# Optimization experiments

Hardware: AMD Instinct MI355X
Metric: run time of the kernel (lower is better)

The kernel has to match this reference:

```python
import jax, jax.numpy as jnp
import numpy as np
from jax import lax

B, C, H, W = 64, 512, 20, 15
N = H * W  # must be 300 (ChannelAttention dim)
EPS = 1e-5


def layernorm(x, w, b):
    m = x.mean(-1, keepdims=True)
    v = x.var(-1, keepdims=True)
    return (x - m) * lax.rsqrt(v + EPS) * w + b


def batchnorm(x, w, b):  # training-mode BN over (B,H,W), x: (B,C,H,W)
    m = x.mean((0, 2, 3), keepdims=True)
    v = x.var((0, 2, 3), keepdims=True)
    return (x - m) * lax.rsqrt(v + EPS) * w[None, :, None, None] + b[None, :, None, None]


def cross_linear_attn(x1, x2, kv1_w, kv2_w, heads):
    # x: (B, n, c); kv_w: (2c, c). Linear-attention variant: softmax over channel axis of k^T v.
    b, n, c = x1.shape
    d = c // heads
    scale = d ** -0.5

    def split_q(x):
        return x.reshape(b, n, heads, d).transpose(0, 2, 1, 3)  # (b,h,n,d)

    def kv(x, w):
        t = (x @ w.T).reshape(b, n, 2, heads, d).transpose(2, 0, 3, 1, 4)
        return t[0], t[1]  # each (b,h,n,d)

    q1, q2 = split_q(x1), split_q(x2)
    k1, v1 = kv(x1, kv1_w)
    k2, v2 = kv(x2, kv2_w)

    def ctx(k, v):  # (b,h,d,d), softmax over dim -2
        return jax.nn.softmax(jnp.einsum('bhnd,bhne->bhde', k, v) * scale, axis=-2)

    c1, c2 = ctx(k1, v1), ctx(k2, v2)

    def out(q, cx):
        return jnp.einsum('bhnd,bhde->bhne', q, cx).transpose(0, 2, 1, 3).reshape(b, n, c)

    return out(q1, c2), out(q2, c1)  # cross: q1 uses ctx2, q2 uses ctx1


def conv1x1(x, w):  # x: (B,Ci,H,W), w: (Co,Ci)
    return jnp.einsum('oi,bihw->bohw', w, x)


def setup_inputs() -> dict:
    key = jax.random.key(0)
    ks = jax.random.split(key, 24)
    g = lambda i, shape, s=0.02: jax.random.normal(ks[i], shape, jnp.float32) * s
    inp = {
        'x1': jax.random.normal(ks[0], (B, C, H, W), jnp.float32),
        'x2': jax.random.normal(ks[1], (B, C, H, W), jnp.float32),
        # CrossPath channel_proj1/2: Linear(C, 2C) + LayerNorm(2C)
        'cp1_w': g(2, (2 * C, C)), 'cp1_b': jnp.zeros((2 * C,), jnp.float32),
        'ln1_w': jnp.ones((2 * C,), jnp.float32), 'ln1_b': jnp.zeros((2 * C,), jnp.float32),
        'cp2_w': g(3, (2 * C, C)), 'cp2_b': jnp.zeros((2 * C,), jnp.float32),
        'ln2_w': jnp.ones((2 * C,), jnp.float32), 'ln2_b': jnp.zeros((2 * C,), jnp.float32),
        # SpatialAttention (dim=C, heads=8) kv linears, no bias
        's_kv1_w': g(4, (2 * C, C)), 's_kv2_w': g(5, (2 * C, C)),
        # ChannelAttention (dim=N=300, heads=4) kv linears, no bias
        'c_kv1_w': g(6, (2 * N, N)), 'c_kv2_w': g(7, (2 * N, N)),
        # ChannelEmbed(2C -> C)
        'res_w': g(8, (C, 2 * C), np.sqrt(2.0 / C)),
        'ce1_w': g(9, (C, 2 * C), np.sqrt(2.0 / C)), 'ce1_b': jnp.zeros((C,), jnp.float32),
        'dw_w': g(10, (C, 1, 3, 3), np.sqrt(2.0 / 9.0)), 'dw_b': jnp.zeros((C,), jnp.float32),
        'ce3_w': g(11, (C, C), np.sqrt(2.0 / C)), 'ce3_b': jnp.zeros((C,), jnp.float32),
        'bn_e_w': jnp.ones((C,), jnp.float32), 'bn_e_b': jnp.zeros((C,), jnp.float32),
        'bn_o_w': jnp.ones((C,), jnp.float32), 'bn_o_b': jnp.zeros((C,), jnp.float32),
    }
    return inp


def reference(x1, x2, cp1_w, cp1_b, ln1_w, ln1_b, cp2_w, cp2_b, ln2_w, ln2_b,
              s_kv1_w, s_kv2_w, c_kv1_w, c_kv2_w,
              res_w, ce1_w, ce1_b, dw_w, dw_b, ce3_w, ce3_b,
              bn_e_w, bn_e_b, bn_o_w, bn_o_b):
    b, c, h, w = x1.shape
    n = h * w
    t1 = x1.reshape(b, c, n).transpose(0, 2, 1)  # (B,N,C)
    t2 = x2.reshape(b, c, n).transpose(0, 2, 1)

    a1 = jax.nn.relu(layernorm(t1 @ cp1_w.T + cp1_b, ln1_w, ln1_b))
    a2 = jax.nn.relu(layernorm(t2 @ cp2_w.T + cp2_b, ln2_w, ln2_b))
    c1, s1 = a1[..., :c], a1[..., c:]
    c2, s2 = a2[..., :c], a2[..., c:]

    v1, v2 = cross_linear_attn(s1, s2, s_kv1_w, s_kv2_w, heads=8)
    z1, z2 = cross_linear_attn(c1.transpose(0, 2, 1), c2.transpose(0, 2, 1),
                               c_kv1_w, c_kv2_w, heads=4)
    s = v1 + v2                                  # (B,N,C)
    cc = (z1 + z2).transpose(0, 2, 1)            # (B,N,C)

    merge = jnp.concatenate([s, cc], axis=-1)    # (B,N,2C)
    xm = merge.transpose(0, 2, 1).reshape(b, 2 * c, h, w)

    residual = conv1x1(xm, res_w)
    e = conv1x1(xm, ce1_w) + ce1_b[None, :, None, None]
    e = lax.conv_general_dilated(e, dw_w, (1, 1), 'SAME',
                                 dimension_numbers=('NCHW', 'OIHW', 'NCHW'),
                                 feature_group_count=c) + dw_b[None, :, None, None]
    e = jnp.where(e >= 0, e, 0.01 * e)  # LeakyReLU(0.01)
    e = conv1x1(e, ce3_w) + ce3_b[None, :, None, None]
    e = batchnorm(e, bn_e_w, bn_e_b)
    return batchnorm(residual + e, bn_o_w, bn_o_b)
```

## Files before the change

### kernel.cpp

```cpp
#include <hip/hip_runtime.h>

typedef unsigned short u16;
typedef __attribute__((ext_vector_type(8))) short bh8;
typedef __attribute__((ext_vector_type(4))) float f4;

__device__ __forceinline__ u16 f2b(float f){
  unsigned int u = __float_as_uint(f);
  u += 0x7fffu + ((u >> 16) & 1u);
  return (u16)(u >> 16);
}
__device__ __forceinline__ float b2f(u16 h){
  return __uint_as_float(((unsigned int)h) << 16);
}
__device__ __forceinline__ void gl16(const u16* g, u16* l){
  __builtin_amdgcn_global_load_lds((const __attribute__((address_space(1))) void*)g,
                                   (__attribute__((address_space(3))) void*)l, 16, 0, 0);
}

__global__ void pack_plain(const float* __restrict__ src, u16* __restrict__ dst, int count){
  int i = blockIdx.x*256 + threadIdx.x;
  if (i < count) dst[i] = f2b(src[i]);
}
__global__ void pack_ckv_k(const float* __restrict__ src, u16* __restrict__ dst){
  int i = blockIdx.x*256 + threadIdx.x;
  int nn = i / 320, kk = i - (i/320)*320;
  int t_ = (nn >= 320) ? 1 : 0;
  int rem = nn - t_*320;
  int hh = rem / 80, dd = rem - hh*80;
  int kh = kk / 80, kd = kk - kh*80;
  float v = 0.f;
  if (dd < 75 && kd < 75)
    v = src[(size_t)(t_*300 + hh*75 + dd)*300 + (kh*75 + kd)];
  dst[i] = f2b(v);
}
__global__ void pack_dw(const float* __restrict__ src, u16* __restrict__ dst){
  int i = blockIdx.x*256 + threadIdx.x;
  if (i < 4608){
    int t = i >> 9, c = i & 511;
    dst[i] = f2b(src[c*9 + t]);
  }
}
__global__ void pad_zero(u16* __restrict__ slack){
  const int j = blockIdx.x*256 + threadIdx.x;
  if (j < 2048) slack[j] = 0;
}

__global__ __launch_bounds__(256)
void transpose_k(const float* __restrict__ x, u16* __restrict__ t)
{
  __shared__ float tile[32][33];
  const int n0 = blockIdx.x * 32, c0 = blockIdx.y * 32, b = blockIdx.z;
  const int ln = threadIdx.x & 31, lr = threadIdx.x >> 5;
  #pragma unroll
  for (int q = 0; q < 4; q++) {
    const int c = c0 + lr + q*8, n = n0 + ln;
    tile[lr + q*8][ln] = (n < 300) ? x[((long)b*512 + c)*300 + n] : 0.f;
  }
  __syncthreads();
  #pragma unroll
  for (int q = 0; q < 4; q++) {
    const int n = n0 + lr + q*8;
    if (n < 300) t[((long)b*300 + n)*512 + c0 + ln] = f2b(tile[ln][lr + q*8]);
  }
}

template<int OUTF, int HASB>
__global__ __launch_bounds__(512)
void gemm_k(const u16* __restrict__ A, int lda,
            const u16* __restrict__ Bw, const u16* __restrict__ Bw2, int ldb, long mhalf,
            u16* __restrict__ Cb, float* __restrict__ Cf, int ldc,
            const float* __restrict__ bias, const float* __restrict__ bias2, int K)
{
  __shared__ u16 As[3][8192];
  __shared__ u16 Bs[3][4096];
  const int tid = threadIdx.x;
  const int gx = gridDim.x;
  const int nwg = gx * gridDim.y;
  const int flat = blockIdx.y * gx + blockIdx.x;
  const int qq = nwg >> 3, rr = nwg & 7, xcd = flat & 7, lin = flat >> 3;
  const int newid = (xcd < rr ? xcd*(qq+1) : rr*(qq+1) + (xcd-rr)*qq) + lin;
  const long n0 = (long)(newid % gx) * 128;
  const long m0 = (long)(newid / gx) * 256;
  const u16* Bwp = Bw; const float* bp = bias;
  if (Bw2 != nullptr && m0 >= mhalf){ Bwp = Bw2; bp = bias2; }
  const int wave = tid >> 6, lane = tid & 63;
  const int l15 = lane & 15, lg = lane >> 4;
  const int wr = (wave >> 1) * 64, wc = (wave & 1) * 64;
  const int arow = tid >> 2;
  const int aseg = ((tid & 3) ^ ((arow >> 1) & 3)) * 8;
  const u16* Ag0 = A + (m0 + arow) * (long)lda + aseg;
  const u16* Ag1 = A + (m0 + 128 + arow) * (long)lda + aseg;
  const u16* Bg0 = Bwp + (n0 + arow) * (long)ldb + aseg;
  const int to8 = tid * 8;
  int roA[4], roB[4];
  #pragma unroll
  for (int i = 0; i < 4; i++){
    const int rA = wr + i*16 + l15;
    roA[i] = rA*32 + ((lg ^ ((rA >> 1) & 3)) * 8);
    const int rB = wc + i*16 + l15;
    roB[i] = rB*32 + ((lg ^ ((rB >> 1) & 3)) * 8);
  }
  f4 acc[4][4] = {};
  const int NT = K >> 5;
  {
    gl16(Ag0, &As[0][to8]); gl16(Ag1, &As[0][4096 + to8]); gl16(Bg0, &Bs[0][to8]);
    gl16(Ag0 + 32, &As[1][to8]); gl16(Ag1 + 32, &As[1][4096 + to8]); gl16(Bg0 + 32, &Bs[1][to8]);
  }
  int rd = 0;
  for (int t = 0; t < NT; t++) {
    if (t < NT - 1) { asm volatile("s_waitcnt vmcnt(3)" ::: "memory"); }
    else            { asm volatile("s_waitcnt vmcnt(0)" ::: "memory"); }
    __builtin_amdgcn_sched_barrier(0);
    __builtin_amdgcn_s_barrier();
    __builtin_amdgcn_sched_barrier(0);
    if (t + 2 < NT) {
      int wb = rd + 2; if (wb >= 3) wb -= 3;
      const int kt = (t + 2) << 5;
      gl16(Ag0 + kt, &As[wb][to8]); gl16(Ag1 + kt, &As[wb][4096 + to8]); gl16(Bg0 + kt, &Bs[wb][to8]);
    }
    bh8 af[4], bf[4];
    #pragma unroll
    for (int mi = 0; mi < 4; mi++) af[mi] = *(const bh8*)&As[rd][roA[mi]];
    #pragma unroll
    for (int ni = 0; ni < 4; ni++) bf[ni] = *(const bh8*)&Bs[rd][roB[ni]];
    #pragma unroll
    for (int mi = 0; mi < 4; mi++)
      #pragma unroll
      for (int ni = 0; ni < 4; ni++)
        acc[mi][ni] = __builtin_amdgcn_mfma_f32_16x16x32_bf16(af[mi], bf[ni], acc[mi][ni], 0, 0, 0);
    rd++; if (rd == 3) rd = 0;
  }
  if (OUTF == 2) {
    if (n0 < 512) {
      #pragma unroll
      for (int ni = 0; ni < 4; ni++) {
        const long cn = n0 + wc + ni*16 + l15;
        #pragma unroll
        for (int mi = 0; mi < 4; mi++)
          #pragma unroll
          for (int r = 0; r < 4; r++) {
            const long cm = m0 + wr + mi*16 + lg*4 + r;
            Cf[cm * ldc + cn] = acc[mi][ni][r];
          }
      }
    } else {
      #pragma unroll
      for (int ni = 0; ni < 4; ni++) {
        const long cn = n0 - 512 + wc + ni*16 + l15;
        const float bv = bias[cn];
        #pragma unroll
        for (int mi = 0; mi < 4; mi++)
          #pragma unroll
          for (int r = 0; r < 4; r++) {
            const long cm = m0 + wr + mi*16 + lg*4 + r;
            Cb[cm * ldc + cn] = f2b(acc[mi][ni][r] + bv);
          }
      }
    }
  } else {
    #pragma unroll
    for (int ni = 0; ni < 4; ni++) {
      const long cn = n0 + wc + ni*16 + l15;
      const float bv = HASB ? bp[cn] : 0.0f;
      #pragma unroll
      for (int mi = 0; mi < 4; mi++) {
        #pragma unroll
        for (int r = 0; r < 4; r++) {
          const long cm = m0 + wr + mi*16 + lg*4 + r;
          const float v = acc[mi][ni][r] + bv;
          if (OUTF) Cf[cm * ldc + cn] = v;
          else      Cb[cm * ldc + cn] = f2b(v);
        }
      }
    }
  }
}

__global__ __launch_bounds__(256)
void ln_kernel(const u16* __restrict__ apre, const float* __restrict__ lw, const float* __restrict__ lb,
               u16* __restrict__ s, u16* __restrict__ cT)
{
  __shared__ u16 tile[40][520];
  const int bh = blockIdx.x;
  const int b = bh >> 2, h = bh & 3;
  const int z = blockIdx.y;
  const int dd0 = z ? 40 : 0;
  const int ndd = z ? 35 : 40;
  const int segbase = z ? 5 : 0;
  const int tid = threadIdx.x, w = tid >> 6, lane = tid & 63;
  const int r0 = b*300 + h*75 + dd0;
  for (int dl = w; dl < ndd; dl += 4){
    const int r = r0 + dl;
    const u16* row = apre + (size_t)r*1024 + lane*8;
    const bh8 vc = *(const bh8*)row;
    const bh8 vs = *(const bh8*)(row + 512);
    float fc[8], fs[8];
    float sm = 0.f, sq = 0.f;
    #pragma unroll
    for (int j = 0; j < 8; j++){
      fc[j] = b2f((u16)vc[j]); fs[j] = b2f((u16)vs[j]);
      sm += fc[j] + fs[j];
      sq += fc[j]*fc[j] + fs[j]*fs[j];
    }
    #pragma unroll
    for (int o = 32; o; o >>= 1){ sm += __shfl_xor(sm, o); sq += __shfl_xor(sq, o); }
    const float mean = sm * (1.f/1024.f);
    const float rstd = rsqrtf(sq*(1.f/1024.f) - mean*mean + 1e-5f);
    bh8 oc, os;
    #pragma unroll
    for (int j = 0; j < 8; j++){
      const int c = lane*8 + j;
      const float y1 = (fc[j]-mean)*rstd*lw[c] + lb[c];
      oc[j] = (short)f2b(fmaxf(y1, 0.f));
      const float y2 = (fs[j]-mean)*rstd*lw[512+c] + lb[512+c];
      os[j] = (short)f2b(fmaxf(y2, 0.f));
    }
    *(bh8*)&tile[dl][lane*8] = oc;
    *(bh8*)&s[(size_t)r*512 + lane*8] = os;
  }
  __syncthreads();
  for (int i = tid; i < 2560; i += 256){
    const int c = i / 5, sg = i - (i/5)*5;
    const int seg = segbase + sg;
    bh8 ov;
    #pragma unroll
    for (int j = 0; j < 8; j++){
      const int dl = seg*8 + j - dd0;
      ov[j] = (short)((dl >= 0 && dl < ndd) ? tile[dl][c] : (u16)0);
    }
    *(bh8*)&cT[((size_t)b*512 + c)*320 + h*80 + seg*8] = ov;
  }
}

template<int D, int DREAL, int OS>
__global__ __launch_bounds__(256)
void ctx_kernel(const u16* __restrict__ kva, const u16* __restrict__ kvb,
                u16* __restrict__ outp, int K, int RS, int VOFF, float scale)
{
  constexpr int NT = D/16, MT = D/16, MTL = (MT+3)/4, SEG = D/8;
  __shared__ u16 vT[D][40];
  __shared__ u16 kT[D][40];
  const int h = blockIdx.x, b = blockIdx.y, iq = blockIdx.z;
  const int Hn = gridDim.x;
  const u16* base = (iq ? kvb : kva) + (size_t)b*K*RS + h*D;
  u16* out = outp + (((size_t)iq*64 + b)*Hn + h)*(size_t)(D*OS);
  const int tid = threadIdx.x, w = tid >> 6, lane = tid & 63, l15 = lane & 15, lg = lane >> 4;
  f4 acc[MTL][NT] = {};
  for (int k0 = 0; k0 < K; k0 += 32) {
    __syncthreads();
    for (int sI = tid; sI < 32*SEG; sI += 256) {
      const int nn = sI / SEG, dseg = sI - (sI/SEG)*SEG;
      bh8 kk = {}, vv = {};
      const int krow = k0 + nn;
      if (krow < K) {
        const u16* p = base + (size_t)krow*RS + dseg*8;
        kk = *(const bh8*)p;
        vv = *(const bh8*)(p + VOFF);
      }
      #pragma unroll
      for (int j = 0; j < 8; j++){
        kT[dseg*8+j][nn] = (u16)kk[j];
        vT[dseg*8+j][nn] = (u16)vv[j];
      }
    }
    __syncthreads();
    #pragma unroll
    for (int ii = 0; ii < MTL; ii++){
      const int mt = w + ii*4;
      if (MT % 4 != 0 && mt >= MT) break;
      const bh8 a = *(const bh8*)&vT[mt*16 + l15][lg*8];
      #pragma unroll
      for (int nt = 0; nt < NT; nt++){
        const bh8 bb = *(const bh8*)&kT[nt*16 + l15][lg*8];
        acc[ii][nt] = __builtin_amdgcn_mfma_f32_16x16x32_bf16(a, bb, acc[ii][nt], 0, 0, 0);
      }
    }
  }
  #pragma unroll
  for (int ii = 0; ii < MTL; ii++){
    const int mt = w + ii*4;
    if (MT % 4 != 0 && mt >= MT) continue;
    #pragma unroll
    for (int r = 0; r < 4; r++){
      const int e = mt*16 + lg*4 + r;
      float xs[NT]; float mx = -1e30f;
      #pragma unroll
      for (int nt = 0; nt < NT; nt++){
        float x = acc[ii][nt][r] * scale;
        if (DREAL != D && (nt*16 + l15) >= DREAL) x = -1e30f;
        xs[nt] = x; mx = fmaxf(mx, x);
      }
      mx = fmaxf(mx, __shfl_xor(mx,1)); mx = fmaxf(mx, __shfl_xor(mx,2));
      mx = fmaxf(mx, __shfl_xor(mx,4)); mx = fmaxf(mx, __shfl_xor(mx,8));
      float smv = 0.f;
      #pragma unroll
      for (int nt = 0; nt < NT; nt++){
        const float p = (xs[nt] > -1e29f) ? __expf(xs[nt]-mx) : 0.f;
        xs[nt] = p; smv += p;
      }
      smv += __shfl_xor(smv,1); smv += __shfl_xor(smv,2);
      smv += __shfl_xor(smv,4); smv += __shfl_xor(smv,8);
      const float inv = 1.f / smv;
      #pragma unroll
      for (int nt = 0; nt < NT; nt++)
        out[(size_t)e*OS + nt*16 + l15] = f2b(xs[nt]*inv);
      if (OS > D) out[(size_t)e*OS + D + l15] = 0;
    }
  }
}

__global__ __launch_bounds__(256)
void sp_out_kernel(const u16* __restrict__ s1, const u16* __restrict__ s2,
                   const u16* __restrict__ csT, u16* __restrict__ merge)
{
  const int h = blockIdx.x, b = blockIdx.y;
  const int tid = threadIdx.x, w = tid >> 6, lane = tid & 63, l15 = lane & 15, lg = lane >> 4;
  const u16* c1 = csT + (((size_t)b)*8 + h)*4096;
  const u16* c2 = csT + (((size_t)64 + b)*8 + h)*4096;
  for (int mt = w; mt < 19; mt += 4) {
    const int m = mt*16 + l15;
    const bool mv = (m < 300);
    const u16* q1 = s1 + ((size_t)b*300 + m)*512 + h*64;
    const u16* q2 = s2 + ((size_t)b*300 + m)*512 + h*64;
    f4 acc[4] = {};
    #pragma unroll
    for (int kc = 0; kc < 2; kc++){
      bh8 a1 = {}, a2 = {};
      if (mv){ a1 = *(const bh8*)(q1 + kc*32 + lg*8); a2 = *(const bh8*)(q2 + kc*32 + lg*8); }
      #pragma unroll
      for (int nt = 0; nt < 4; nt++){
        const bh8 b2v = *(const bh8*)&c2[(size_t)(nt*16+l15)*64 + kc*32 + lg*8];
        acc[nt] = __builtin_amdgcn_mfma_f32_16x16x32_bf16(a1, b2v, acc[nt], 0, 0, 0);
        const bh8 b1v = *(const bh8*)&c1[(size_t)(nt*16+l15)*64 + kc*32 + lg*8];
        acc[nt] = __builtin_amdgcn_mfma_f32_16x16x32_bf16(a2, b1v, acc[nt], 0, 0, 0);
      }
    }
    #pragma unroll
    for (int nt = 0; nt < 4; nt++)
      #pragma unroll
      for (int r = 0; r < 4; r++){
        const int mm = mt*16 + lg*4 + r;
        if (mm < 300)
          merge[((size_t)b*300 + mm)*1024 + h*64 + nt*16 + l15] = f2b(acc[nt][r]);
      }
  }
}

__global__ __launch_bounds__(256)
void ch_out_kernel(const u16* __restrict__ cT1, const u16* __restrict__ cT2,
                   const u16* __restrict__ ccT, u16* __restrict__ merge)
{
  const int cb = blockIdx.x, h = blockIdx.y, b = blockIdx.z;
  const int tid = threadIdx.x, w = tid >> 6, lane = tid & 63, l15 = lane & 15, lg = lane >> 4;
  const int chbase = cb*128 + w*32;
  f4 acc[5][2] = {};
  #pragma unroll
  for (int oi = 0; oi < 2; oi++){
    const u16* Am = ccT + (((size_t)((oi==0)?1:0)*64 + b)*4 + h)*(size_t)(80*96);
    const u16* qb = (oi==0) ? cT1 : cT2;
    #pragma unroll
    for (int kc = 0; kc < 3; kc++){
      bh8 bf[2];
      #pragma unroll
      for (int nf = 0; nf < 2; nf++){
        const int ch = chbase + nf*16 + l15;
        bf[nf] = *(const bh8*)&qb[((size_t)b*512 + ch)*320 + h*80 + kc*32 + lg*8];
      }
      #pragma unroll
      for (int mt = 0; mt < 5; mt++){
        const bh8 a = *(const bh8*)&Am[(size_t)(mt*16+l15)*96 + kc*32 + lg*8];
        #pragma unroll
        for (int nf = 0; nf < 2; nf++)
          acc[mt][nf] = __builtin_amdgcn_mfma_f32_16x16x32_bf16(a, bf[nf], acc[mt][nf], 0, 0, 0);
      }
    }
  }
  #pragma unroll
  for (int mt = 0; mt < 5; mt++)
    #pragma unroll
    for (int nf = 0; nf < 2; nf++)
      #pragma unroll
      for (int r = 0; r < 4; r++){
        const int e = mt*16 + lg*4 + r;
        if (e < 75)
          merge[((size_t)b*300 + h*75 + e)*1024 + 512 + chbase + nf*16 + l15] = f2b(acc[mt][nf][r]);
      }
}

__global__ __launch_bounds__(256)
void dw_kernel(const u16* __restrict__ e1, const u16* __restrict__ dwt,
               const float* __restrict__ bias, u16* __restrict__ d1)
{
  const int idx = blockIdx.x*256 + threadIdx.x;
  const int cg = idx & 63;
  const int sp = (idx >> 6) % 300;
  const int b  = idx / (64*300);
  const int c0 = cg*8;
  const int hh = sp / 15, ww = sp - hh*15;
  float acc[8];
  {
    const float4 b0 = *(const float4*)&bias[c0];
    const float4 b1 = *(const float4*)&bias[c0+4];
    acc[0]=b0.x; acc[1]=b0.y; acc[2]=b0.z; acc[3]=b0.w;
    acc[4]=b1.x; acc[5]=b1.y; acc[6]=b1.z; acc[7]=b1.w;
  }
  #pragma unroll
  for (int dy = -1; dy <= 1; dy++){
    const int h2 = hh + dy; if (h2 < 0 || h2 >= 20) continue;
    #pragma unroll
    for (int dx = -1; dx <= 1; dx++){
      const int w2 = ww + dx; if (w2 < 0 || w2 >= 15) continue;
      const bh8 vv = *(const bh8*)&e1[((size_t)b*300 + h2*15 + w2)*512 + c0];
      const int t = (dy+1)*3 + (dx+1);
      const bh8 wv = *(const bh8*)&dwt[t*512 + c0];
      #pragma unroll
      for (int j = 0; j < 8; j++)
        acc[j] += b2f((u16)vv[j]) * b2f((u16)wv[j]);
    }
  }
  bh8 ov;
  #pragma unroll
  for (int j = 0; j < 8; j++){
    float y = acc[j];
    y = (y >= 0.f) ? y : 0.01f*y;
    ov[j] = (short)f2b(y);
  }
  *(bh8*)&d1[((size_t)b*300 + sp)*512 + c0] = ov;
}

__global__ __launch_bounds__(256)
void stats_k(const float* __restrict__ e3, const float* __restrict__ res, float* __restrict__ st){
  const int tid = threadIdx.x;
  const int c0 = tid*2;
  const size_t r0 = (size_t)blockIdx.x * 128;
  float se0=0,se1=0,qe0=0,qe1=0,sr0=0,sr1=0,qr0=0,qr1=0,x0=0,x1=0;
  for (int rr = 0; rr < 128; rr++){
    const size_t o2 = (r0+rr)*512 + c0;
    const float2 ev = *(const float2*)&e3[o2];
    const float2 rv = *(const float2*)&res[o2];
    se0 += ev.x; se1 += ev.y; qe0 += ev.x*ev.x; qe1 += ev.y*ev.y;
    sr0 += rv.x; sr1 += rv.y; qr0 += rv.x*rv.x; qr1 += rv.y*rv.y;
    x0  += ev.x*rv.x; x1 += ev.y*rv.y;
  }
  atomicAdd(&st[c0], se0);      atomicAdd(&st[c0+1], se1);
  atomicAdd(&st[512+c0], qe0);  atomicAdd(&st[512+c0+1], qe1);
  atomicAdd(&st[1024+c0], sr0); atomicAdd(&st[1024+c0+1], sr1);
  atomicAdd(&st[1536+c0], qr0); atomicAdd(&st[1536+c0+1], qr1);
  atomicAdd(&st[2048+c0], x0);  atomicAdd(&st[2048+c0+1], x1);
}
__global__ void fin_k(float* st, const float* __restrict__ we, const float* __restrict__ be,
                      const float* __restrict__ wo, const float* __restrict__ bo){
  const int c = threadIdx.x;
  const float Nf = 19200.f, iN = 1.f/19200.f;
  const float Se = st[c], Qe = st[512+c], Sr = st[1024+c], Qr = st[1536+c], X = st[2048+c];
  const float me = Se*iN;
  const float ve = Qe*iN - me*me;
  const float ae = we[c]*rsqrtf(ve + 1e-5f);
  const float bev = be[c] - me*ae;
  const float So = Sr + ae*Se + Nf*bev;
  const float Qo = Qr + ae*ae*Qe + Nf*bev*bev + 2.f*ae*X + 2.f*bev*Sr + 2.f*ae*bev*Se;
  const float mo = So*iN;
  const float vo = Qo*iN - mo*mo;
  const float ao = wo[c]*rsqrtf(vo + 1e-5f);
  const float bov = bo[c] - mo*ao;
  st[2560+c] = ae; st[3072+c] = bev; st[3584+c] = ao; st[4096+c] = bov;
}
__global__ __launch_bounds__(256)
void final_kernel(const float* __restrict__ res, const float* __restrict__ e3,
                  const float* __restrict__ st, float* __restrict__ outp)
{
  __shared__ float tile[64][65];
  const int spt = blockIdx.x, cht = blockIdx.y, b = blockIdx.z;
  const int tid = threadIdx.x;
  const int sp0 = spt*64, ch0 = cht*64;
  for (int idx = tid; idx < 4096; idx += 256){
    const int cl = idx & 63, sl = idx >> 6;
    const int sp = sp0 + sl;
    float v = 0.f;
    if (sp < 300){
      const size_t off = ((size_t)b*300 + sp)*512 + ch0 + cl;
      const int c = ch0 + cl;
      const float e = e3[off]*st[2560+c] + st[3072+c];
      v = (res[off] + e)*st[3584+c] + st[4096+c];
    }
    tile[sl][cl] = v;
  }
  __syncthreads();
  for (int idx = tid; idx < 4096; idx += 256){
    const int sl = idx & 63, cl = idx >> 6;
    const int sp = sp0 + sl;
    if (sp < 300)
      outp[((size_t)b*512 + ch0 + cl)*300 + sp] = tile[sl][cl];
  }
}

extern "C" void kernel_launch(void* const* d_in, const int* in_sizes, int n_in,
                              void* d_out, int out_size, void* d_ws, size_t ws_size,
                              hipStream_t stream)
{
  const float* x1    = (const float*)d_in[0];
  const float* x2    = (const float*)d_in[1];
  const float* cp1_w = (const float*)d_in[2];
  const float* cp1_b = (const float*)d_in[3];
  const float* ln1_w = (const float*)d_in[4];
  const float* ln1_b = (const float*)d_in[5];
  const float* cp2_w = (const float*)d_in[6];
  const float* cp2_b = (const float*)d_in[7];
  const float* ln2_w = (const float*)d_in[8];
  const float* ln2_b = (const float*)d_in[9];
  const float* skv1w = (const float*)d_in[10];
  const float* skv2w = (const float*)d_in[11];
  const float* ckv1w = (const float*)d_in[12];
  const float* ckv2w = (const float*)d_in[13];
  const float* resw  = (const float*)d_in[14];
  const float* ce1w  = (const float*)d_in[15];
  const float* ce1b  = (const float*)d_in[16];
  const float* dww   = (const float*)d_in[17];
  const float* dwb   = (const float*)d_in[18];
  const float* ce3w  = (const float*)d_in[19];
  const float* ce3b  = (const float*)d_in[20];
  const float* bnew  = (const float*)d_in[21];
  const float* bneb  = (const float*)d_in[22];
  const float* bnow  = (const float*)d_in[23];
  const float* bnob  = (const float*)d_in[24];
  float* out = (float*)d_out;
  char* ws = (char*)d_ws;

  const size_t SZ_T    = (size_t)19200*512*2;
  const size_t SZ_APRE = (size_t)19200*1024*2;
  const size_t SZ_CKV  = (size_t)32768*640*2;
  const size_t SZ_CT   = (size_t)64*512*320*2;
  const size_t SZ_F32  = (size_t)19200*512*4;

  size_t off = 0;
  auto AL = [&](size_t sz){ size_t r = off; off += (sz + 255) & ~(size_t)255; return r; };
  const size_t oR0 = AL(2*SZ_T);
  const size_t oR1 = AL(2*SZ_CKV);
  const size_t oR2 = AL(2*SZ_T);
  const size_t oR3 = AL(2*SZ_CT + 4096);
  const size_t oR4 = AL(SZ_F32);
  const size_t oR5 = AL((size_t)2*64*8*64*64*2);
  const size_t oR6 = AL((size_t)2*64*4*80*96*2);
  const size_t oWcp1  = AL((size_t)1024*512*2);
  const size_t oWcp2  = AL((size_t)1024*512*2);
  const size_t oWskv1 = AL((size_t)1024*512*2);
  const size_t oWskv2 = AL((size_t)1024*512*2);
  const size_t oWckv1 = AL((size_t)640*320*2);
  const size_t oWckv2 = AL((size_t)640*320*2);
  const size_t oWresce = AL((size_t)1024*1024*2);
  const size_t oWce3  = AL((size_t)512*512*2);
  const size_t oWdw   = AL((size_t)9*512*2);
  const size_t oST    = AL(20480);
  (void)ws_size; (void)in_sizes; (void)n_in; (void)out_size;

  u16* t1    = (u16*)(ws + oR0);
  u16* merge = (u16*)(ws + oR0);
  u16* apre1 = (u16*)(ws + oR1);
  u16* ckv1  = (u16*)(ws + oR1);
  u16* s1    = (u16*)(ws + oR2);
  u16* s2    = (u16*)(ws + oR2 + SZ_T);
  u16* e1    = s1;
  u16* d1    = s2;
  u16* cT1   = (u16*)(ws + oR3);
  u16* cT2   = (u16*)(ws + oR3 + SZ_CT);
  u16* slack = (u16*)(ws + oR3 + 2*SZ_CT);
  float* e3  = (float*)(ws + oR3);
  float* resb = (float*)(ws + oR4);
  u16* csT   = (u16*)(ws + oR5);
  u16* ccT   = (u16*)(ws + oR6);
  u16* wcp1  = (u16*)(ws + oWcp1);
  u16* wcp2  = (u16*)(ws + oWcp2);
  u16* wskv1 = (u16*)(ws + oWskv1);
  u16* wskv2 = (u16*)(ws + oWskv2);
  u16* wckv1 = (u16*)(ws + oWckv1);
  u16* wckv2 = (u16*)(ws + oWckv2);
  u16* wresce = (u16*)(ws + oWresce);
  u16* wce3  = (u16*)(ws + oWce3);
  u16* wdw   = (u16*)(ws + oWdw);
  float* st  = (float*)(ws + oST);

  u16* t2    = t1 + 19200*512;
  u16* kv1   = apre1;
  u16* ckv2  = ckv1 + (size_t)32768*640;

  hipMemsetAsync(st, 0, 10240, stream);
  pad_zero<<<8,256,0,stream>>>(slack);
  pack_plain<<<2048,256,0,stream>>>(cp1_w, wcp1, 524288);
  pack_plain<<<2048,256,0,stream>>>(cp2_w, wcp2, 524288);
  pack_plain<<<2048,256,0,stream>>>(skv1w, wskv1, 524288);
  pack_plain<<<2048,256,0,stream>>>(skv2w, wskv2, 524288);
  pack_ckv_k<<<800,256,0,stream>>>(ckv1w, wckv1);
  pack_ckv_k<<<800,256,0,stream>>>(ckv2w, wckv2);
  pack_plain<<<2048,256,0,stream>>>(resw, wresce, 524288);
  pack_plain<<<2048,256,0,stream>>>(ce1w, wresce + 524288, 524288);
  pack_plain<<<1024,256,0,stream>>>(ce3w, wce3, 262144);
  pack_dw<<<18,256,0,stream>>>(dww, wdw);

  transpose_k<<<dim3(10,16,64),256,0,stream>>>(x1, t1);
  transpose_k<<<dim3(10,16,64),256,0,stream>>>(x2, t2);

  gemm_k<0,1><<<dim3(8,150),512,0,stream>>>(t1,512, wcp1,wcp2,512, 19200L,
                                            apre1,nullptr,1024, cp1_b,cp2_b, 512);

  ln_kernel<<<dim3(256,2),256,0,stream>>>(apre1, ln1_w, ln1_b, s1, cT1);
  ln_kernel<<<dim3(256,2),256,0,stream>>>(apre1 + (size_t)19200*1024, ln2_w, ln2_b, s2, cT2);

  gemm_k<0,0><<<dim3(8,150),512,0,stream>>>(s1,512, wskv1,wskv2,512, 19200L,
                                            kv1,nullptr,1024, nullptr,nullptr, 512);

  ctx_kernel<64,64,64><<<dim3(8,64,2),256,0,stream>>>(kv1, kv1 + (size_t)19200*1024, csT, 300, 1024, 512, 0.125f);

  gemm_k<0,0><<<dim3(5,256),512,0,stream>>>(cT1,320, wckv1,wckv2,320, 32768L,
                                            ckv1,nullptr,640, nullptr,nullptr, 320);

  ctx_kernel<80,75,96><<<dim3(4,64,2),256,0,stream>>>(ckv1, ckv2, ccT, 512, 640, 320, 0.115470054f);

  sp_out_kernel<<<dim3(8,64),256,0,stream>>>(s1, s2, csT, merge);
  ch_out_kernel<<<dim3(4,4,64),256,0,stream>>>(cT1, cT2, ccT, merge);

  gemm_k<2,0><<<dim3(8,75),512,0,stream>>>(merge,1024, wresce,nullptr,1024, (long)1<<40,
                                           e1, resb, 512, ce1b,nullptr, 1024);

  dw_kernel<<<4800,256,0,stream>>>(e1, wdw, dwb, d1);

  gemm_k<1,1><<<dim3(4,75),512,0,stream>>>(d1,512, wce3,nullptr,512, (long)1<<40,
                                           nullptr,e3,512, ce3b,nullptr, 512);

  stats_k<<<150,256,0,stream>>>(e3, resb, st);
  fin_k<<<1,512,0,stream>>>(st, bnew, bneb, bnow, bnob);
  final_kernel<<<dim3(5,8,64),256,0,stream>>>(resb, e3, st, out);
}
```

Measured before the change: 544.1 us.

## Add 256x256-tile GEMM kernel and store residual/e3 intermediates as bf16

```diff
diff --git a/kernel.cpp b/kernel.cpp
--- a/kernel.cpp
+++ b/kernel.cpp
@@ -61,6 +61,132 @@
   for (int q = 0; q < 4; q++) {
     const int n = n0 + lr + q*8;
     if (n < 300) t[((long)b*300 + n)*512 + c0 + ln] = f2b(tile[ln][lr + q*8]);
+  }
+}
+
+template<int OUTF, int HASB>
+__global__ __launch_bounds__(512, 2)
+void gemm256(const u16* __restrict__ A, int lda,
+             const u16* __restrict__ Bw, const u16* __restrict__ Bw2, int ldb, long mhalf,
+             u16* __restrict__ Cb, float* __restrict__ Cf, int ldc,
+             const float* __restrict__ bias, const float* __restrict__ bias2, int K)
+{
+  __shared__ u16 As[2][16384];
+  __shared__ u16 Bs[2][16384];
+  const int tid = threadIdx.x;
+  const int gx = gridDim.x;
+  const int nwg = gx * gridDim.y;
+  const int flat = blockIdx.y * gx + blockIdx.x;
+  const int qq = nwg >> 3, rr = nwg & 7, xcd = flat & 7, lin = flat >> 3;
+  const int newid = (xcd < rr ? xcd*(qq+1) : rr*(qq+1) + (xcd-rr)*qq) + lin;
+  const long n0 = (long)(newid % gx) * 256;
+  const long m0 = (long)(newid / gx) * 256;
+  const u16* Bwp = Bw; const float* bp = bias;
+  if (Bw2 != nullptr && m0 >= mhalf){ Bwp = Bw2; bp = bias2; }
+  const int wave = tid >> 6, lane = tid & 63;
+  const int l15 = lane & 15, lg = lane >> 4;
+  const int wr = (wave >> 2) * 128;
+  const int wc = (wave & 3) * 64;
+  const int srow = tid >> 3;
+  const int gseg = ((tid & 7) ^ (srow & 7)) * 8;
+  const u16* Ag[4]; const u16* Bg[4];
+  #pragma unroll
+  for (int q = 0; q < 4; q++){
+    Ag[q] = A   + (m0 + q*64 + srow) * (long)lda + gseg;
+    Bg[q] = Bwp + (n0 + q*64 + srow) * (long)ldb + gseg;
+  }
+  int roA[8], roB[4];
+  #pragma unroll
+  for (int i = 0; i < 8; i++){ const int rA = wr + i*16 + l15; roA[i] = rA*64 + ((lg ^ (rA & 7)) * 8); }
+  #pragma unroll
+  for (int i = 0; i < 4; i++){ const int rB = wc + i*16 + l15; roB[i] = rB*64 + ((lg ^ (rB & 7)) * 8); }
+  f4 acc[8][4] = {};
+  const int NT = K >> 6;
+  #pragma unroll
+  for (int q = 0; q < 4; q++){
+    gl16(Ag[q], &As[0][(q*512 + tid)*8]);
+    gl16(Bg[q], &Bs[0][(q*512 + tid)*8]);
+  }
+  asm volatile("s_waitcnt vmcnt(0)" ::: "memory");
+  __builtin_amdgcn_sched_barrier(0);
+  __builtin_amdgcn_s_barrier();
+  __builtin_amdgcn_sched_barrier(0);
+  int cur = 0;
+  for (int t = 0; t < NT; t++) {
+    if (t + 1 < NT) {
+      const int kt = (t + 1) << 6;
+      const int nb = cur ^ 1;
+      #pragma unroll
+      for (int q = 0; q < 4; q++){
+        gl16(Ag[q] + kt, &As[nb][(q*512 + tid)*8]);
+        gl16(Bg[q] + kt, &Bs[nb][(q*512 + tid)*8]);
+      }
+    }
+    #pragma unroll
+    for (int ks = 0; ks < 2; ks++){
+      const int kx = ks * 32;
+      bh8 af[8], bf[4];
+      #pragma unroll
+      for (int mi = 0; mi < 8; mi++) af[mi] = *(const bh8*)&As[cur][roA[mi] ^ kx];
+      #pragma unroll
+      for (int ni = 0; ni < 4; ni++) bf[ni] = *(const bh8*)&Bs[cur][roB[ni] ^ kx];
+      __builtin_amdgcn_s_setprio(1);
+      #pragma unroll
+      for (int mi = 0; mi < 8; mi++)
+        #pragma unroll
+        for (int ni = 0; ni < 4; ni++)
+          acc[mi][ni] = __builtin_amdgcn_mfma_f32_16x16x32_bf16(af[mi], bf[ni], acc[mi][ni], 0, 0, 0);
+      __builtin_amdgcn_s_setprio(0);
+    }
+    if (t + 1 < NT) {
+      asm volatile("s_waitcnt vmcnt(0)" ::: "memory");
+      __builtin_amdgcn_sched_barrier(0);
+      __builtin_amdgcn_s_barrier();
+      __builtin_amdgcn_sched_barrier(0);
+      cur ^= 1;
+    }
+  }
+  if (OUTF == 2) {
+    u16* resb16 = (u16*)Cf;
+    if (n0 < 512) {
+      #pragma unroll
+      for (int ni = 0; ni < 4; ni++) {
+        const long cn = n0 + wc + ni*16 + l15;
+        #pragma unroll
+        for (int mi = 0; mi < 8; mi++)
+          #pragma unroll
+          for (int r = 0; r < 4; r++) {
+            const long cm = m0 + wr + mi*16 + lg*4 + r;
+            resb16[cm * ldc + cn] = f2b(acc[mi][ni][r]);
+          }
+      }
+    } else {
+      #pragma unroll
+      for (int ni = 0; ni < 4; ni++) {
+        const long cn = n0 - 512 + wc + ni*16 + l15;
+        const float bv = bias[cn];
+        #pragma unroll
+        for (int mi = 0; mi < 8; mi++)
+          #pragma unroll
+          for (int r = 0; r < 4; r++) {
+            const long cm = m0 + wr + mi*16 + lg*4 + r;
+            Cb[cm * ldc + cn] = f2b(acc[mi][ni][r] + bv);
+          }
+      }
+    }
+  } else {
+    #pragma unroll
+    for (int ni = 0; ni < 4; ni++) {
+      const long cn = n0 + wc + ni*16 + l15;
+      const float bv = HASB ? bp[cn] : 0.0f;
+      #pragma unroll
+      for (int mi = 0; mi < 8; mi++)
+        #pragma unroll
+        for (int r = 0; r < 4; r++) {
+          const long cm = m0 + wr + mi*16 + lg*4 + r;
+          Cb[cm * ldc + cn] = f2b(acc[mi][ni][r] + bv);
+        }
+    }
   }
 }
 
@@ -130,47 +256,18 @@
         acc[mi][ni] = __builtin_amdgcn_mfma_f32_16x16x32_bf16(af[mi], bf[ni], acc[mi][ni], 0, 0, 0);
     rd++; if (rd == 3) rd = 0;
   }
-  if (OUTF == 2) {
-    if (n0 < 512) {
-      #pragma unroll
-      for (int ni = 0; ni < 4; ni++) {
-        const long cn = n0 + wc + ni*16 + l15;
-        #pragma unroll
-        for (int mi = 0; mi < 4; mi++)
-          #pragma unroll
-          for (int r = 0; r < 4; r++) {
-            const long cm = m0 + wr + mi*16 + lg*4 + r;
-            Cf[cm * ldc + cn] = acc[mi][ni][r];
-          }
-      }
-    } else {
-      #pragma unroll
-      for (int ni = 0; ni < 4; ni++) {
-        const long cn = n0 - 512 + wc + ni*16 + l15;
-        const float bv = bias[cn];
-        #pragma unroll
-        for (int mi = 0; mi < 4; mi++)
-          #pragma unroll
-          for (int r = 0; r < 4; r++) {
-            const long cm = m0 + wr + mi*16 + lg*4 + r;
-            Cb[cm * ldc + cn] = f2b(acc[mi][ni][r] + bv);
-          }
-      }
-    }
-  } else {
-    #pragma unroll
-    for (int ni = 0; ni < 4; ni++) {
-      const long cn = n0 + wc + ni*16 + l15;
-      const float bv = HASB ? bp[cn] : 0.0f;
-      #pragma unroll
-      for (int mi = 0; mi < 4; mi++) {
-        #pragma unroll
-        for (int r = 0; r < 4; r++) {
-          const long cm = m0 + wr + mi*16 + lg*4 + r;
-          const float v = acc[mi][ni][r] + bv;
-          if (OUTF) Cf[cm * ldc + cn] = v;
-          else      Cb[cm * ldc + cn] = f2b(v);
-        }
+  #pragma unroll
+  for (int ni = 0; ni < 4; ni++) {
+    const long cn = n0 + wc + ni*16 + l15;
+    const float bv = HASB ? bp[cn] : 0.0f;
+    #pragma unroll
+    for (int mi = 0; mi < 4; mi++) {
+      #pragma unroll
+      for (int r = 0; r < 4; r++) {
+        const long cm = m0 + wr + mi*16 + lg*4 + r;
+        const float v = acc[mi][ni][r] + bv;
+        if (OUTF) Cf[cm * ldc + cn] = v;
+        else      Cb[cm * ldc + cn] = f2b(v);
       }
     }
   }
@@ -429,18 +526,20 @@
 }
 
 __global__ __launch_bounds__(256)
-void stats_k(const float* __restrict__ e3, const float* __restrict__ res, float* __restrict__ st){
+void stats_k(const u16* __restrict__ e3, const u16* __restrict__ res, float* __restrict__ st){
   const int tid = threadIdx.x;
   const int c0 = tid*2;
   const size_t r0 = (size_t)blockIdx.x * 128;
   float se0=0,se1=0,qe0=0,qe1=0,sr0=0,sr1=0,qr0=0,qr1=0,x0=0,x1=0;
   for (int rr = 0; rr < 128; rr++){
     const size_t o2 = (r0+rr)*512 + c0;
-    const float2 ev = *(const float2*)&e3[o2];
-    const float2 rv = *(const float2*)&res[o2];
-    se0 += ev.x; se1 += ev.y; qe0 += ev.x*ev.x; qe1 += ev.y*ev.y;
-    sr0 += rv.x; sr1 += rv.y; qr0 += rv.x*rv.x; qr1 += rv.y*rv.y;
-    x0  += ev.x*rv.x; x1 += ev.y*rv.y;
+    const unsigned int eu = *(const unsigned int*)&e3[o2];
+    const unsigned int ru = *(const unsigned int*)&res[o2];
+    const float ex = b2f((u16)(eu & 0xffff)), ey = b2f((u16)(eu >> 16));
+    const float rx = b2f((u16)(ru & 0xffff)), ry = b2f((u16)(ru >> 16));
+    se0 += ex; se1 += ey; qe0 += ex*ex; qe1 += ey*ey;
+    sr0 += rx; sr1 += ry; qr0 += rx*rx; qr1 += ry*ry;
+    x0  += ex*rx; x1 += ey*ry;
   }
   atomicAdd(&st[c0], se0);      atomicAdd(&st[c0+1], se1);
   atomicAdd(&st[512+c0], qe0);  atomicAdd(&st[512+c0+1], qe1);
@@ -466,24 +565,28 @@
   st[2560+c] = ae; st[3072+c] = bev; st[3584+c] = ao; st[4096+c] = bov;
 }
 __global__ __launch_bounds__(256)
-void final_kernel(const float* __restrict__ res, const float* __restrict__ e3,
+void final_kernel(const u16* __restrict__ res, const u16* __restrict__ e3,
                   const float* __restrict__ st, float* __restrict__ outp)
 {
   __shared__ float tile[64][65];
   const int spt = blockIdx.x, cht = blockIdx.y, b = blockIdx.z;
   const int tid = threadIdx.x;
   const int sp0 = spt*64, ch0 = cht*64;
-  for (int idx = tid; idx < 4096; idx += 256){
-    const int cl = idx & 63, sl = idx >> 6;
+  for (int idx = tid; idx < 2048; idx += 256){
+    const int cl = (idx & 31)*2, sl = idx >> 5;
     const int sp = sp0 + sl;
-    float v = 0.f;
+    float v0 = 0.f, v1 = 0.f;
     if (sp < 300){
       const size_t off = ((size_t)b*300 + sp)*512 + ch0 + cl;
       const int c = ch0 + cl;
-      const float e = e3[off]*st[2560+c] + st[3072+c];
-      v = (res[off] + e)*st[3584+c] + st[4096+c];
-    }
-    tile[sl][cl] = v;
+      const unsigned int eu = *(const unsigned int*)&e3[off];
+      const unsigned int ru = *(const unsigned int*)&res[off];
+      const float e0 = b2f((u16)(eu & 0xffff))*st[2560+c]   + st[3072+c];
+      const float e1 = b2f((u16)(eu >> 16))   *st[2560+c+1] + st[3072+c+1];
+      v0 = (b2f((u16)(ru & 0xffff)) + e0)*st[3584+c]   + st[4096+c];
+      v1 = (b2f((u16)(ru >> 16))    + e1)*st[3584+c+1] + st[4096+c+1];
+    }
+    tile[sl][cl] = v0; tile[sl][cl+1] = v1;
   }
   __syncthreads();
   for (int idx = tid; idx < 4096; idx += 256){
@@ -564,8 +667,8 @@
   u16* cT1   = (u16*)(ws + oR3);
   u16* cT2   = (u16*)(ws + oR3 + SZ_CT);
   u16* slack = (u16*)(ws + oR3 + 2*SZ_CT);
-  float* e3  = (float*)(ws + oR3);
-  float* resb = (float*)(ws + oR4);
+  u16* e3b   = (u16*)(ws + oR3);
+  u16* resb  = (u16*)(ws + oR4);
   u16* csT   = (u16*)(ws + oR5);
   u16* ccT   = (u16*)(ws + oR6);
   u16* wcp1  = (u16*)(ws + oWcp1);
@@ -599,14 +702,14 @@
   transpose_k<<<dim3(10,16,64),256,0,stream>>>(x1, t1);
   transpose_k<<<dim3(10,16,64),256,0,stream>>>(x2, t2);
 
-  gemm_k<0,1><<<dim3(8,150),512,0,stream>>>(t1,512, wcp1,wcp2,512, 19200L,
-                                            apre1,nullptr,1024, cp1_b,cp2_b, 512);
+  gemm256<0,1><<<dim3(4,150),512,0,stream>>>(t1,512, wcp1,wcp2,512, 19200L,
+                                             apre1,nullptr,1024, cp1_b,cp2_b, 512);
 
   ln_kernel<<<dim3(256,2),256,0,stream>>>(apre1, ln1_w, ln1_b, s1, cT1);
   ln_kernel<<<dim3(256,2),256,0,stream>>>(apre1 + (size_t)19200*1024, ln2_w, ln2_b, s2, cT2);
 
-  gemm_k<0,0><<<dim3(8,150),512,0,stream>>>(s1,512, wskv1,wskv2,512, 19200L,
-                                            kv1,nullptr,1024, nullptr,nullptr, 512);
+  gemm256<0,0><<<dim3(4,150),512,0,stream>>>(s1,512, wskv1,wskv2,512, 19200L,
+                                             kv1,nullptr,1024, nullptr,nullptr, 512);
 
   ctx_kernel<64,64,64><<<dim3(8,64,2),256,0,stream>>>(kv1, kv1 + (size_t)19200*1024, csT, 300, 1024, 512, 0.125f);
 
@@ -618,15 +721,15 @@
   sp_out_kernel<<<dim3(8,64),256,0,stream>>>(s1, s2, csT, merge);
   ch_out_kernel<<<dim3(4,4,64),256,0,stream>>>(cT1, cT2, ccT, merge);
 
-  gemm_k<2,0><<<dim3(8,75),512,0,stream>>>(merge,1024, wresce,nullptr,1024, (long)1<<40,
-                                           e1, resb, 512, ce1b,nullptr, 1024);
+  gemm256<2,0><<<dim3(4,75),512,0,stream>>>(merge,1024, wresce,nullptr,1024, (long)1<<40,
+                                            e1, (float*)resb, 512, ce1b,nullptr, 1024);
 
   dw_kernel<<<4800,256,0,stream>>>(e1, wdw, dwb, d1);
 
-  gemm_k<1,1><<<dim3(4,75),512,0,stream>>>(d1,512, wce3,nullptr,512, (long)1<<40,
-                                           nullptr,e3,512, ce3b,nullptr, 512);
-
-  stats_k<<<150,256,0,stream>>>(e3, resb, st);
+  gemm_k<0,1><<<dim3(4,75),512,0,stream>>>(d1,512, wce3,nullptr,512, (long)1<<40,
+                                           e3b,nullptr,512, ce3b,nullptr, 512);
+
+  stats_k<<<150,256,0,stream>>>(e3b, resb, st);
   fin_k<<<1,512,0,stream>>>(st, bnew, bneb, bnow, bnob);
-  final_kernel<<<dim3(5,8,64),256,0,stream>>>(resb, e3, st, out);
-}
+  final_kernel<<<dim3(5,8,64),256,0,stream>>>(resb, e3b, st, out);
+}
```

Result: slower. 558.3 us (+2.6%).

## Store residual and ce3 outputs as bf16 and raise MFMA wave priority

Applied to the files above, without the earlier changes.

```diff
diff --git a/kernel.cpp b/kernel.cpp
--- a/kernel.cpp
+++ b/kernel.cpp
@@ -123,14 +123,17 @@
     for (int mi = 0; mi < 4; mi++) af[mi] = *(const bh8*)&As[rd][roA[mi]];
     #pragma unroll
     for (int ni = 0; ni < 4; ni++) bf[ni] = *(const bh8*)&Bs[rd][roB[ni]];
+    __builtin_amdgcn_s_setprio(1);
     #pragma unroll
     for (int mi = 0; mi < 4; mi++)
       #pragma unroll
       for (int ni = 0; ni < 4; ni++)
         acc[mi][ni] = __builtin_amdgcn_mfma_f32_16x16x32_bf16(af[mi], bf[ni], acc[mi][ni], 0, 0, 0);
+    __builtin_amdgcn_s_setprio(0);
     rd++; if (rd == 3) rd = 0;
   }
   if (OUTF == 2) {
+    u16* resb16 = (u16*)Cf;
     if (n0 < 512) {
       #pragma unroll
       for (int ni = 0; ni < 4; ni++) {
@@ -140,7 +143,7 @@
           #pragma unroll
           for (int r = 0; r < 4; r++) {
             const long cm = m0 + wr + mi*16 + lg*4 + r;
-            Cf[cm * ldc + cn] = acc[mi][ni][r];
+            resb16[cm * ldc + cn] = f2b(acc[mi][ni][r]);
           }
       }
     } else {
@@ -167,9 +170,7 @@
         #pragma unroll
         for (int r = 0; r < 4; r++) {
           const long cm = m0 + wr + mi*16 + lg*4 + r;
-          const float v = acc[mi][ni][r] + bv;
-          if (OUTF) Cf[cm * ldc + cn] = v;
-          else      Cb[cm * ldc + cn] = f2b(v);
+          Cb[cm * ldc + cn] = f2b(acc[mi][ni][r] + bv);
         }
       }
     }
@@ -429,18 +430,20 @@
 }
 
 __global__ __launch_bounds__(256)
-void stats_k(const float* __restrict__ e3, const float* __restrict__ res, float* __restrict__ st){
+void stats_k(const u16* __restrict__ e3, const u16* __restrict__ res, float* __restrict__ st){
   const int tid = threadIdx.x;
   const int c0 = tid*2;
   const size_t r0 = (size_t)blockIdx.x * 128;
   float se0=0,se1=0,qe0=0,qe1=0,sr0=0,sr1=0,qr0=0,qr1=0,x0=0,x1=0;
   for (int rr = 0; rr < 128; rr++){
     const size_t o2 = (r0+rr)*512 + c0;
-    const float2 ev = *(const float2*)&e3[o2];
-    const float2 rv = *(const float2*)&res[o2];
-    se0 += ev.x; se1 += ev.y; qe0 += ev.x*ev.x; qe1 += ev.y*ev.y;
-    sr0 += rv.x; sr1 += rv.y; qr0 += rv.x*rv.x; qr1 += rv.y*rv.y;
-    x0  += ev.x*rv.x; x1 += ev.y*rv.y;
+    const unsigned int eu = *(const unsigned int*)&e3[o2];
+    const unsigned int ru = *(const unsigned int*)&res[o2];
+    const float ex = b2f((u16)(eu & 0xffff)), ey = b2f((u16)(eu >> 16));
+    const float rx = b2f((u16)(ru & 0xffff)), ry = b2f((u16)(ru >> 16));
+    se0 += ex; se1 += ey; qe0 += ex*ex; qe1 += ey*ey;
+    sr0 += rx; sr1 += ry; qr0 += rx*rx; qr1 += ry*ry;
+    x0  += ex*rx; x1 += ey*ry;
   }
   atomicAdd(&st[c0], se0);      atomicAdd(&st[c0+1], se1);
   atomicAdd(&st[512+c0], qe0);  atomicAdd(&st[512+c0+1], qe1);
@@ -466,24 +469,28 @@
   st[2560+c] = ae; st[3072+c] = bev; st[3584+c] = ao; st[4096+c] = bov;
 }
 __global__ __launch_bounds__(256)
-void final_kernel(const float* __restrict__ res, const float* __restrict__ e3,
+void final_kernel(const u16* __restrict__ res, const u16* __restrict__ e3,
                   const float* __restrict__ st, float* __restrict__ outp)
 {
   __shared__ float tile[64][65];
   const int spt = blockIdx.x, cht = blockIdx.y, b = blockIdx.z;
   const int tid = threadIdx.x;
   const int sp0 = spt*64, ch0 = cht*64;
-  for (int idx = tid; idx < 4096; idx += 256){
-    const int cl = idx & 63, sl = idx >> 6;
+  for (int idx = tid; idx < 2048; idx += 256){
+    const int cl = (idx & 31)*2, sl = idx >> 5;
     const int sp = sp0 + sl;
-    float v = 0.f;
+    float v0 = 0.f, v1 = 0.f;
     if (sp < 300){
       const size_t off = ((size_t)b*300 + sp)*512 + ch0 + cl;
       const int c = ch0 + cl;
-      const float e = e3[off]*st[2560+c] + st[3072+c];
-      v = (res[off] + e)*st[3584+c] + st[4096+c];
-    }
-    tile[sl][cl] = v;
+      const unsigned int eu = *(const unsigned int*)&e3[off];
+      const unsigned int ru = *(const unsigned int*)&res[off];
+      const float e0 = b2f((u16)(eu & 0xffff))*st[2560+c]   + st[3072+c];
+      const float e1 = b2f((u16)(eu >> 16))   *st[2560+c+1] + st[3072+c+1];
+      v0 = (b2f((u16)(ru & 0xffff)) + e0)*st[3584+c]   + st[4096+c];
+      v1 = (b2f((u16)(ru >> 16))    + e1)*st[3584+c+1] + st[4096+c+1];
+    }
+    tile[sl][cl] = v0; tile[sl][cl+1] = v1;
   }
   __syncthreads();
   for (int idx = tid; idx < 4096; idx += 256){
@@ -564,8 +571,8 @@
   u16* cT1   = (u16*)(ws + oR3);
   u16* cT2   = (u16*)(ws + oR3 + SZ_CT);
   u16* slack = (u16*)(ws + oR3 + 2*SZ_CT);
-  float* e3  = (float*)(ws + oR3);
-  float* resb = (float*)(ws + oR4);
+  u16* e3b   = (u16*)(ws + oR3);
+  u16* resb  = (u16*)(ws + oR4);
   u16* csT   = (u16*)(ws + oR5);
   u16* ccT   = (u16*)(ws + oR6);
   u16* wcp1  = (u16*)(ws + oWcp1);
@@ -619,14 +626,14 @@
   ch_out_kernel<<<dim3(4,4,64),256,0,stream>>>(cT1, cT2, ccT, merge);
 
   gemm_k<2,0><<<dim3(8,75),512,0,stream>>>(merge,1024, wresce,nullptr,1024, (long)1<<40,
-                                           e1, resb, 512, ce1b,nullptr, 1024);
+                                           e1, (float*)resb, 512, ce1b,nullptr, 1024);
 
   dw_kernel<<<4800,256,0,stream>>>(e1, wdw, dwb, d1);
 
-  gemm_k<1,1><<<dim3(4,75),512,0,stream>>>(d1,512, wce3,nullptr,512, (long)1<<40,
-                                           nullptr,e3,512, ce3b,nullptr, 512);
-
-  stats_k<<<150,256,0,stream>>>(e3, resb, st);
+  gemm_k<0,1><<<dim3(4,75),512,0,stream>>>(d1,512, wce3,nullptr,512, (long)1<<40,
+                                           e3b,nullptr,512, ce3b,nullptr, 512);
+
+  stats_k<<<150,256,0,stream>>>(e3b, resb, st);
   fin_k<<<1,512,0,stream>>>(st, bnew, bneb, bnow, bnob);
-  final_kernel<<<dim3(5,8,64),256,0,stream>>>(resb, e3, st, out);
-}
+  final_kernel<<<dim3(5,8,64),256,0,stream>>>(resb, e3b, st, out);
+}
```

Result: faster. 525.3 us (-3.5%).
